# Optimization experiments

Measured on AMD Instinct MI355X. Metric: run time of the kernel, lower is better.

## Reference

```python
import jax, jax.numpy as jnp
import numpy as np

S, Q, N, T, G = 20000, 32, 200000, 30, 64
D_IN, H, D_SV, D_LANG, D_FUSE = 300, 256, 64, 64, 128

def setup_inputs() -> dict:
    key = jax.random.key(0)
    ks = jax.random.split(key, 20)
    sc = 0.05
    inp = {
        'lang_feat': jax.random.normal(ks[0], (Q, T, D_IN), jnp.float32),
        'supvox_feat': jax.random.normal(ks[1], (S, D_SV), jnp.float32),
        'supvox_coords': jax.random.uniform(ks[2], (S, 3), jnp.float32),
        'lang_len': jax.random.randint(ks[3], (Q,), 5, T + 1).astype(jnp.int32),
        'grps': jax.random.randint(ks[4], (S,), 0, G).astype(jnp.int32),
        'supervox': jax.random.randint(ks[5], (N,), 0, S).astype(jnp.int32),
        'gt': jax.random.randint(ks[6], (N, Q), 0, 2).astype(jnp.int32),
        # GRU params (torch layout: [3H, in])
        'gru_w_ih': sc * jax.random.normal(ks[7], (3 * H, D_IN), jnp.float32),
        'gru_w_hh': sc * jax.random.normal(ks[8], (3 * H, H), jnp.float32),
        'gru_b_ih': sc * jax.random.normal(ks[9], (3 * H,), jnp.float32),
        'gru_b_hh': sc * jax.random.normal(ks[10], (3 * H,), jnp.float32),
        # lang_sqz: Linear(256,64) ReLU Linear(64,64)
        'sqz_w1': sc * jax.random.normal(ks[11], (D_LANG, H), jnp.float32),
        'sqz_b1': sc * jax.random.normal(ks[12], (D_LANG,), jnp.float32),
        'sqz_w2': sc * jax.random.normal(ks[13], (D_LANG, D_LANG), jnp.float32),
        'sqz_b2': sc * jax.random.normal(ks[14], (D_LANG,), jnp.float32),
        # feat_fuse: Linear(131,128) ReLU
        'fuse_w': sc * jax.random.normal(ks[15], (D_FUSE, D_SV + 3 + D_LANG), jnp.float32),
        'fuse_b': sc * jax.random.normal(ks[16], (D_FUSE,), jnp.float32),
        # heat_map: Linear(128,2) (Dropout = identity in eval)
        'heat_w': sc * jax.random.normal(ks[17], (2, D_FUSE), jnp.float32),
        'heat_b': sc * jax.random.normal(ks[18], (2,), jnp.float32),
    }
    return inp

def _gru_last(x, lens, w_ih, w_hh, b_ih, b_hh):
    # x: [Q, T, D_IN]; returns hidden at step lens[q]-1 (pack_padded_sequence semantics)
    def step(h, xt_t):
        xt, t = xt_t  # xt: [Q, D_IN]
        gi = xt @ w_ih.T + b_ih          # [Q, 3H]
        gh = h @ w_hh.T + b_hh           # [Q, 3H]
        ir, iz, inn = jnp.split(gi, 3, -1)
        hr, hz, hn = jnp.split(gh, 3, -1)
        r = jax.nn.sigmoid(ir + hr)
        z = jax.nn.sigmoid(iz + hz)
        n = jnp.tanh(inn + r * hn)
        h_new = (1.0 - z) * n + z * h
        h = jnp.where((t < lens)[:, None], h_new, h)
        return h, None
    h0 = jnp.zeros((x.shape[0], w_hh.shape[1]), x.dtype)
    hT, _ = jax.lax.scan(step, h0, (jnp.swapaxes(x, 0, 1), jnp.arange(x.shape[1])))
    return hT  # [Q, H]

def reference(lang_feat, supvox_feat, supvox_coords, lang_len, grps, supervox, gt,
              gru_w_ih, gru_w_hh, gru_b_ih, gru_b_hh,
              sqz_w1, sqz_b1, sqz_w2, sqz_b2, fuse_w, fuse_b, heat_w, heat_b):
    # language branch
    h = _gru_last(lang_feat, lang_len, gru_w_ih, gru_w_hh, gru_b_ih, gru_b_hh)  # [Q,H]
    lang = jax.nn.relu(h @ sqz_w1.T + sqz_b1) @ sqz_w2.T + sqz_b2               # [Q,64]
    # supervoxel branch: cat(feat, coords) -> [S,67]
    sv = jnp.concatenate([supvox_feat, supvox_coords], -1)
    # feat_fuse on cat(sv, lang): split the weight to avoid materializing [S,Q,131]
    d_sv = sv.shape[-1]
    sv_proj = sv @ fuse_w[:, :d_sv].T           # [S,128]
    lang_proj = lang @ fuse_w[:, d_sv:].T       # [Q,128]
    fused = jax.nn.relu(sv_proj[:, None, :] + lang_proj[None, :, :] + fuse_b)  # [S,Q,128]
    logits = fused @ heat_w.T + heat_b          # [S,Q,2]
    obj_score = jax.nn.softmax(logits, -1)[..., 1]  # [S,Q]
    # cluster-grouped mean score (grps_ one-hot; assumes unique(grps)==arange(G))
    grp_oh = (grps[:, None] == jnp.arange(G)).astype(obj_score.dtype)  # [S,G]
    grp_sum = jnp.einsum('sq,sg->qg', obj_score, grp_oh)               # [Q,G]
    sen_grp_score = grp_sum / grp_oh.sum(0)[None, :]                   # [Q,G]
    best = jnp.argmax(sen_grp_score, -1)        # [Q]
    supvox_sen = grp_oh[:, best]                # [S,Q] binary
    obj_pts = supvox_sen[supervox].astype(jnp.int32)  # [N,Q]
    inter = (obj_pts * gt).sum(0).astype(jnp.float32)
    union = jnp.bitwise_or(obj_pts, gt).sum(0).astype(jnp.float32)
    ious = inter / (union + 1e-5)               # [Q]
    return obj_pts, ious
```

## Files before the change

### kernel.cpp

```cpp
#include <hip/hip_runtime.h>
#include <hip/hip_bf16.h>
#include <math.h>

#define S_TOT 20000
#define Q_TOT 32
#define N_TOT 200000
#define T_MAX 30
#define G_TOT 64
#define D_IN 300
#define H_DIM 256
#define D_SV 64
#define D_LANG 64
#define D_FUSE 128
#define D_CAT 67
#define FW_LD 131
#define SCHUNK 32
#define NBLK3 (S_TOT / SCHUNK)
#define SENT64 0xFFFFFFFFFFFFFFFFull
#define OUT_GRID 2048
#define PCHUNK 16
#define PTILES 40

#define GI_MT 32
#define GI_NT 64
#define GI_KC 100
#define GI_NB 12
#define GI_GRID (30 * GI_NB)
#define HG_ELEMS (30 * Q_TOT * H_DIM)

#define SYNCS_N 160

__device__ __forceinline__ float sigmoidf_(float x) { return 1.0f / (1.0f + expf(-x)); }
__device__ __forceinline__ unsigned long long pack2(float a, float b) {
    return ((unsigned long long)__float_as_uint(b) << 32) | (unsigned long long)__float_as_uint(a);
}

__global__ __launch_bounds__(128) void k_gi(const float* __restrict__ lang_feat,
                                            const float* __restrict__ w_ih,
                                            const float* __restrict__ b_ih,
                                            const float* __restrict__ fuse_w,
                                            const float* __restrict__ sqz_w1,
                                            const float* __restrict__ sqz_w2,
                                            const float* __restrict__ heat_w,
                                            float* __restrict__ gi,
                                            float* __restrict__ fwt,
                                            float* __restrict__ w1t,
                                            float* __restrict__ w2t,
                                            float* __restrict__ wdr,
                                            float* __restrict__ hg,
                                            int* __restrict__ syncs) {
    const int tid = threadIdx.x;
    if (blockIdx.x >= GI_GRID) {
        const int xb = blockIdx.x - GI_GRID;
        if (xb == 0) {
            for (int i = tid; i < FW_LD * D_FUSE; i += 128)
                fwt[(i % FW_LD) * D_FUSE + (i / FW_LD)] = fuse_w[i];
            for (int i = tid; i < D_LANG * H_DIM; i += 128)
                w1t[(i & 255) * D_LANG + (i >> 8)] = sqz_w1[i];
            for (int i = tid; i < D_LANG * D_LANG; i += 128)
                w2t[(i & 63) * D_LANG + (i >> 6)] = sqz_w2[i];
            if (tid < D_FUSE) wdr[tid] = heat_w[D_FUSE + tid] - heat_w[tid];
        } else {
            const int fb = xb - 1;
            const int per4 = HG_ELEMS / 4 / 8;
            float4* dst = (float4*)hg + fb * per4;
            const float4 sv = make_float4(__uint_as_float(0xFFFFFFFFu), __uint_as_float(0xFFFFFFFFu),
                                          __uint_as_float(0xFFFFFFFFu), __uint_as_float(0xFFFFFFFFu));
            for (int i = tid; i < per4; i += 128) dst[i] = sv;
            if (fb == 0) for (int i = tid; i < SYNCS_N; i += 128) syncs[i] = 0;
        }
        return;
    }
    __shared__ float x_l[GI_KC][GI_MT + 1];
    __shared__ float w_l[GI_KC][GI_NT + 1];
    const int mb = blockIdx.x / GI_NB, nb = blockIdx.x % GI_NB;
    const int m0 = mb * GI_MT, n0 = nb * GI_NT;
    const int tq4 = (tid >> 4) * 4, jq4 = (tid & 15) * 4;

    float acc[4][4];
    #pragma unroll
    for (int i = 0; i < 4; ++i)
        #pragma unroll
        for (int j = 0; j < 4; ++j) acc[i][j] = 0.f;

    for (int kc = 0; kc < 3; ++kc) {
        const int k0 = kc * GI_KC;
        for (int i = tid; i < GI_MT * GI_KC; i += 128) {
            const int r = i / GI_KC, k = i % GI_KC;
            const int row = m0 + r, q = row / T_MAX, t = row - q * T_MAX;
            x_l[k][r] = lang_feat[(q * T_MAX + t) * D_IN + k0 + k];
        }
        for (int i = tid; i < GI_NT * GI_KC; i += 128) {
            const int r = i / GI_KC, k = i % GI_KC;
            w_l[k][r] = w_ih[(n0 + r) * D_IN + k0 + k];
        }
        __syncthreads();
        #pragma unroll 2
        for (int k = 0; k < GI_KC; ++k) {
            const float x0 = x_l[k][tq4 + 0], x1 = x_l[k][tq4 + 1];
            const float x2 = x_l[k][tq4 + 2], x3 = x_l[k][tq4 + 3];
            const float v0 = w_l[k][jq4 + 0], v1 = w_l[k][jq4 + 1];
            const float v2 = w_l[k][jq4 + 2], v3 = w_l[k][jq4 + 3];
            acc[0][0] = fmaf(x0, v0, acc[0][0]); acc[0][1] = fmaf(x0, v1, acc[0][1]);
            acc[0][2] = fmaf(x0, v2, acc[0][2]); acc[0][3] = fmaf(x0, v3, acc[0][3]);
            acc[1][0] = fmaf(x1, v0, acc[1][0]); acc[1][1] = fmaf(x1, v1, acc[1][1]);
            acc[1][2] = fmaf(x1, v2, acc[1][2]); acc[1][3] = fmaf(x1, v3, acc[1][3]);
            acc[2][0] = fmaf(x2, v0, acc[2][0]); acc[2][1] = fmaf(x2, v1, acc[2][1]);
            acc[2][2] = fmaf(x2, v2, acc[2][2]); acc[2][3] = fmaf(x2, v3, acc[2][3]);
            acc[3][0] = fmaf(x3, v0, acc[3][0]); acc[3][1] = fmaf(x3, v1, acc[3][1]);
            acc[3][2] = fmaf(x3, v2, acc[3][2]); acc[3][3] = fmaf(x3, v3, acc[3][3]);
        }
        __syncthreads();
    }
    const float b0 = b_ih[n0 + jq4 + 0], b1 = b_ih[n0 + jq4 + 1];
    const float b2 = b_ih[n0 + jq4 + 2], b3 = b_ih[n0 + jq4 + 3];
    #pragma unroll
    for (int i = 0; i < 4; ++i) {
        const int row = m0 + tq4 + i;
        const int q = row / T_MAX, t = row - q * T_MAX;
        float4 v = make_float4(acc[i][0] + b0, acc[i][1] + b1, acc[i][2] + b2, acc[i][3] + b3);
        *(float4*)&gi[(q * T_MAX + t) * 768 + n0 + jq4] = v;
    }
}

__global__ __launch_bounds__(384, 1) void k_gru8(const float* __restrict__ gi,
                                                 const float* __restrict__ w_hh,
                                                 const float* __restrict__ b_hh,
                                                 const int* __restrict__ lang_len,
                                                 float* __restrict__ hg,
                                                 float* __restrict__ hbuf,
                                                 const float* __restrict__ w1t,
                                                 const float* __restrict__ b1,
                                                 const float* __restrict__ w2t,
                                                 const float* __restrict__ b2,
                                                 const float* __restrict__ fwt,
                                                 const float* __restrict__ fuse_b,
                                                 float* __restrict__ langc,
                                                 int* __restrict__ qdone) {
    __shared__ __align__(16) float wlds[96 * 256];
    __shared__ __align__(16) float hlq[4 * 68];
    __shared__ float ghl[96];
    __shared__ float gil[T_MAX * 96];

    const int tid = threadIdx.x;
    const int q = blockIdx.x >> 3, b = blockIdx.x & 7;
    int len = lang_len[q]; if (len > T_MAX) len = T_MAX; if (len < 1) len = 1;

    {
        const float4* src4 = (const float4*)w_hh;
        float4* dst4 = (float4*)wlds;
        for (int i = tid; i < 96 * 64; i += 384) {
            const int r = i >> 6, c = i & 63;
            const int grow = ((r >> 5) << 8) + (b << 5) + (r & 31);
            dst4[r * 64 + (c ^ (r & 7))] = src4[grow * 64 + c];
        }
    }
    for (int i = tid; i < len * 96; i += 384) {
        const int t = i / 96, r = i % 96;
        gil[i] = gi[(q * T_MAX + t) * 768 + ((r >> 5) << 8) + (b << 5) + (r & 31)];
    }
    __syncthreads();

    float hfin = 0.f;
    {
        float hnew = 0.f;
        if (tid < 32) {
            const float bhr = b_hh[(b << 5) + tid];
            const float bhz = b_hh[H_DIM + (b << 5) + tid];
            const float bhn = b_hh[2 * H_DIM + (b << 5) + tid];
            const float r = sigmoidf_(gil[tid] + bhr);
            const float z = sigmoidf_(gil[32 + tid] + bhz);
            const float n = tanhf(gil[64 + tid] + r * bhn);
            hnew = (1.f - z) * n;
            if (len == 1) hfin = hnew;
        }
        if (tid < 64 && len > 1) {
            const float a0 = __shfl(hnew, 2 * (tid & 15));
            const float a1 = __shfl(hnew, 2 * (tid & 15) + 1);
            if (tid < 16) {
                unsigned long long* dst = (unsigned long long*)(hg + q * H_DIM + (b << 5));
                __hip_atomic_store(dst + tid, pack2(a0, a1), __ATOMIC_RELAXED, __HIP_MEMORY_SCOPE_AGENT);
            }
        }
    }

    const int row = tid >> 2, ql = tid & 3;
    const float bh = b_hh[((row >> 5) << 8) + (b << 5) + (row & 31)];
    const int rx = row & 7;
    const float4* wrow4 = (const float4*)wlds + row * 64;
    const int cbase = ql << 4;

    for (int t = 1; t < len; ++t) {
        if (tid < 128) {
            const unsigned long long* src =
                (const unsigned long long*)(hg + (size_t)(t - 1) * (Q_TOT * H_DIM) + q * H_DIM);
            unsigned long long v;
            while ((v = __hip_atomic_load(src + tid, __ATOMIC_RELAXED,
                                          __HIP_MEMORY_SCOPE_AGENT)) == SENT64)
                __builtin_amdgcn_s_sleep(1);
            const int k = 2 * tid;
            const int o = (k >> 6) * 68 + (k & 63);
            hlq[o]     = __uint_as_float((unsigned)(v & 0xffffffffu));
            hlq[o + 1] = __uint_as_float((unsigned)(v >> 32));
        }
        __syncthreads();
        float hold = 0.f;
        if (tid < 32) { const int k = (b << 5) + tid; hold = hlq[(k >> 6) * 68 + (k & 63)]; }
        const float4* h4 = (const float4*)(hlq + ql * 68);
        float ax = 0.f, ay = 0.f, az = 0.f, aw = 0.f;
        #pragma unroll
        for (int i = 0; i < 16; ++i) {
            const float4 wv = wrow4[(cbase + i) ^ rx];
            const float4 hv = h4[i];
            ax = fmaf(wv.x, hv.x, ax);
            ay = fmaf(wv.y, hv.y, ay);
            az = fmaf(wv.z, hv.z, az);
            aw = fmaf(wv.w, hv.w, aw);
        }
        float s = (ax + ay) + (az + aw);
        s += __shfl_xor(s, 1);
        s += __shfl_xor(s, 2);
        if (ql == 0) ghl[row] = s + bh;
        __syncthreads();
        float hnew = 0.f;
        if (tid < 32) {
            const float* gt_ = gil + t * 96;
            const float r = sigmoidf_(gt_[tid] + ghl[tid]);
            const float z = sigmoidf_(gt_[32 + tid] + ghl[32 + tid]);
            const float n = tanhf(gt_[64 + tid] + r * ghl[64 + tid]);
            hnew = (1.f - z) * n + z * hold;
            if (t == len - 1) hfin = hnew;
        }
        if (tid < 64 && t < len - 1) {
            const float a0 = __shfl(hnew, 2 * (tid & 15));
            const float a1 = __shfl(hnew, 2 * (tid & 15) + 1);
            if (tid < 16) {
                unsigned long long* dst =
                    (unsigned long long*)(hg + (size_t)t * (Q_TOT * H_DIM) + q * H_DIM + (b << 5));
                __hip_atomic_store(dst + tid, pack2(a0, a1), __ATOMIC_RELAXED, __HIP_MEMORY_SCOPE_AGENT);
            }
        }
    }

    if (tid < 32)
        __hip_atomic_store(&hbuf[q * H_DIM + (b << 5) + tid], hfin,
                           __ATOMIC_RELAXED, __HIP_MEMORY_SCOPE_AGENT);
    asm volatile("s_waitcnt vmcnt(0)" ::: "memory");
    __syncthreads();
    if (tid == 0)
        __hip_atomic_fetch_add(&qdone[q], 1, __ATOMIC_RELAXED, __HIP_MEMORY_SCOPE_AGENT);
    if (b != 0) return;

    if (tid == 0) {
        while (__hip_atomic_load(&qdone[q], __ATOMIC_RELAXED, __HIP_MEMORY_SCOPE_AGENT) < 8)
            __builtin_amdgcn_s_sleep(2);
    }
    __syncthreads();
    float* hql = gil;
    float* t1l = gil + 256;
    float* lgl = gil + 320;
    if (tid < H_DIM)
        hql[tid] = __hip_atomic_load(&hbuf[q * H_DIM + tid], __ATOMIC_RELAXED, __HIP_MEMORY_SCOPE_AGENT);
    __syncthreads();
    if (tid < 256) {
        const int c = tid >> 2, qq = tid & 3;
        float a = 0.f;
        #pragma unroll 8
        for (int j = 0; j < 64; ++j) {
            const int k = (qq << 6) + j;
            a = fmaf(w1t[k * D_LANG + c], hql[k], a);
        }
        a += __shfl_xor(a, 1);
        a += __shfl_xor(a, 2);
        if (qq == 0) t1l[c] = fmaxf(a + b1[c], 0.f);
    }
    __syncthreads();
    if (tid < 256) {
        const int c = tid >> 2, qq = tid & 3;
        float a = 0.f;
        #pragma unroll
        for (int j = 0; j < 16; ++j) {
            const int k = (qq << 4) + j;
            a = fmaf(w2t[k * D_LANG + c], t1l[k], a);
        }
        a += __shfl_xor(a, 1);
        a += __shfl_xor(a, 2);
        if (qq == 0) lgl[c] = a + b2[c];
    }
    __syncthreads();
    if (tid < 256) {
        const int d = tid >> 1, hh = tid & 1;
        float a = 0.f;
        #pragma unroll 8
        for (int j = 0; j < 32; ++j) {
            const int k = (hh << 5) + j;
            a = fmaf(fwt[(D_CAT + k) * D_FUSE + d], lgl[k], a);
        }
        a += __shfl_xor(a, 1);
        if (hh == 0) langc[q * D_FUSE + d] = a + fuse_b[d];
    }
}

__global__ __launch_bounds__(256) void k_fuse(const float* __restrict__ feat,
                                              const float* __restrict__ coords,
                                              const int* __restrict__ grps,
                                              const float* __restrict__ langc,
                                              const float* __restrict__ fwt,
                                              const float* __restrict__ wdr_g,
                                              const float* __restrict__ heat_b,
                                              float* __restrict__ grp_part,
                                              int* __restrict__ cnt_part) {
    __shared__ __align__(16) float svin[SCHUNK][68];
    __shared__ __align__(16) float svp[SCHUNK][132];
    __shared__ float score[SCHUNK][Q_TOT];
    __shared__ int grps_l[SCHUNK];
    const int tid = threadIdx.x;
    const int s0 = blockIdx.x * SCHUNK;

    const int dsl = tid & 7, q = tid >> 3;
    float lc[16], wdr[16];
    #pragma unroll
    for (int i = 0; i < 16; ++i) {
        const int d = dsl * 16 + i;
        lc[i]  = langc[q * D_FUSE + d];
        wdr[i] = wdr_g[d];
    }
    const float hbd = heat_b[1] - heat_b[0];

    for (int i = tid; i < SCHUNK * D_SV; i += 256) {
        const int r = i >> 6, c = i & 63;
        svin[r][c] = feat[(s0 + r) * D_SV + c];
    }
    if (tid < SCHUNK * 3) { const int r = tid / 3, c = tid % 3; svin[r][D_SV + c] = coords[(s0 + r) * 3 + c]; }
    if (tid < SCHUNK) grps_l[tid] = grps[s0 + tid];
    __syncthreads();

    {
        const int d = tid & 127, sl0 = tid >> 7;
        float acc[16];
        #pragma unroll
        for (int i = 0; i < 16; ++i) acc[i] = 0.f;
        for (int k4 = 0; k4 < 16; ++k4) {
            const float w0 = fwt[(4 * k4 + 0) * D_FUSE + d];
            const float w1 = fwt[(4 * k4 + 1) * D_FUSE + d];
            const float w2 = fwt[(4 * k4 + 2) * D_FUSE + d];
            const float w3 = fwt[(4 * k4 + 3) * D_FUSE + d];
            #pragma unroll
            for (int i = 0; i < 16; ++i) {
                const float4 xv = *(const float4*)&svin[sl0 + 2 * i][4 * k4];
                acc[i] = fmaf(xv.x, w0, fmaf(xv.y, w1, fmaf(xv.z, w2, fmaf(xv.w, w3, acc[i]))));
            }
        }
        for (int k = 64; k < D_CAT; ++k) {
            const float wv = fwt[k * D_FUSE + d];
            #pragma unroll
            for (int i = 0; i < 16; ++i)
                acc[i] = fmaf(svin[sl0 + 2 * i][k], wv, acc[i]);
        }
        #pragma unroll
        for (int i = 0; i < 16; ++i) svp[sl0 + 2 * i][d] = acc[i];
    }
    __syncthreads();

    for (int sl = 0; sl < SCHUNK; ++sl) {
        const float4* sv4 = (const float4*)(&svp[sl][dsl * 16]);
        float part = 0.f;
        #pragma unroll
        for (int j = 0; j < 4; ++j) {
            const float4 v = sv4[j];
            part = fmaf(fmaxf(v.x + lc[4*j+0], 0.f), wdr[4*j+0], part);
            part = fmaf(fmaxf(v.y + lc[4*j+1], 0.f), wdr[4*j+1], part);
            part = fmaf(fmaxf(v.z + lc[4*j+2], 0.f), wdr[4*j+2], part);
            part = fmaf(fmaxf(v.w + lc[4*j+3], 0.f), wdr[4*j+3], part);
        }
        part += __shfl_xor(part, 1);
        part += __shfl_xor(part, 2);
        part += __shfl_xor(part, 4);
        if (dsl == 0) score[sl][q] = sigmoidf_(part + hbd);
    }
    __syncthreads();

    for (int i = 0; i < 8; ++i) {
        const int cell = tid + 256 * i;
        const int qq = cell >> 6, g = cell & 63;
        float sum = 0.f;
        #pragma unroll
        for (int sl = 0; sl < SCHUNK; ++sl)
            sum += (grps_l[sl] == g) ? score[sl][qq] : 0.f;
        grp_part[blockIdx.x * (Q_TOT * G_TOT) + cell] = sum;
        if (cell < G_TOT) {
            int c = 0;
            #pragma unroll
            for (int sl = 0; sl < SCHUNK; ++sl) c += (grps_l[sl] == g);
            cnt_part[blockIdx.x * G_TOT + g] = c;
        }
    }
}

__global__ __launch_bounds__(256) void k_post(const float* __restrict__ grp_part,
                                              const int* __restrict__ cnt_part,
                                              const int* __restrict__ grps,
                                              float* __restrict__ grp2,
                                              int* __restrict__ cnt2,
                                              int* __restrict__ best,
                                              int* __restrict__ smask,
                                              int* __restrict__ qtick,
                                              int* __restrict__ gtick) {
    __shared__ float ps[4][G_TOT];
    __shared__ int   pc[4][G_TOT];
    __shared__ float sc[G_TOT];
    __shared__ int bl[Q_TOT];
    __shared__ int myturn, lastq;
    const int tid = threadIdx.x;
    const int q = blockIdx.x & 31, c = blockIdx.x >> 5;
    const int bq = tid >> 6, g = tid & 63;
    const int b0 = c * PTILES;
    int b1 = b0 + PTILES; if (b1 > NBLK3) b1 = NBLK3;

    float acc = 0.f; int cacc = 0;
    for (int b = b0 + bq; b < b1; b += 4) {
        acc  += grp_part[b * (Q_TOT * G_TOT) + q * G_TOT + g];
        cacc += cnt_part[b * G_TOT + g];
    }
    ps[bq][g] = acc; pc[bq][g] = cacc;
    __syncthreads();
    if (tid < G_TOT) {
        const float s = ((ps[0][tid] + ps[1][tid]) + ps[2][tid]) + ps[3][tid];
        const int  cc = ((pc[0][tid] + pc[1][tid]) + pc[2][tid]) + pc[3][tid];
        __hip_atomic_store(&grp2[(c * Q_TOT + q) * G_TOT + tid], s,
                           __ATOMIC_RELAXED, __HIP_MEMORY_SCOPE_AGENT);
        __hip_atomic_store(&cnt2[(c * Q_TOT + q) * G_TOT + tid], cc,
                           __ATOMIC_RELAXED, __HIP_MEMORY_SCOPE_AGENT);
    }
    asm volatile("s_waitcnt vmcnt(0)" ::: "memory");
    if (tid == 0) {
        const int old = __hip_atomic_fetch_add(&qtick[q], 1, __ATOMIC_RELAXED, __HIP_MEMORY_SCOPE_AGENT);
        myturn = (old == PCHUNK - 1) ? 1 : 0;
    }
    __syncthreads();
    if (!myturn) return;

    if (tid < G_TOT) {
        float s = 0.f; int cc = 0;
        #pragma unroll
        for (int c2 = 0; c2 < PCHUNK; ++c2) {
            s  += __hip_atomic_load(&grp2[(c2 * Q_TOT + q) * G_TOT + tid],
                                    __ATOMIC_RELAXED, __HIP_MEMORY_SCOPE_AGENT);
            cc += __hip_atomic_load(&cnt2[(c2 * Q_TOT + q) * G_TOT + tid],
                                    __ATOMIC_RELAXED, __HIP_MEMORY_SCOPE_AGENT);
        }
        sc[tid] = s / (float)cc;
    }
    __syncthreads();
    if (tid == 0) {
        float bv = sc[0]; int bi = 0;
        for (int g2 = 1; g2 < G_TOT; ++g2) if (sc[g2] > bv) { bv = sc[g2]; bi = g2; }
        __hip_atomic_store(&best[q], bi, __ATOMIC_RELAXED, __HIP_MEMORY_SCOPE_AGENT);
        asm volatile("s_waitcnt vmcnt(0)" ::: "memory");
        const int old = __hip_atomic_fetch_add(gtick, 1, __ATOMIC_RELAXED, __HIP_MEMORY_SCOPE_AGENT);
        lastq = (old == Q_TOT - 1) ? 1 : 0;
    }
    __syncthreads();
    if (!lastq) return;
    if (tid < Q_TOT) bl[tid] = __hip_atomic_load(&best[tid], __ATOMIC_RELAXED, __HIP_MEMORY_SCOPE_AGENT);
    __syncthreads();
    for (int s = tid; s < S_TOT; s += 256) {
        const int gg = grps[s];
        int m = 0;
        #pragma unroll
        for (int qq = 0; qq < Q_TOT; ++qq) m |= (bl[qq] == gg) ? (1 << qq) : 0;
        smask[s] = m;
    }
}

__global__ __launch_bounds__(256) void k_out(const int* __restrict__ supervox,
                                             const int* __restrict__ gt,
                                             const int* __restrict__ smask,
                                             float* __restrict__ out,
                                             int* __restrict__ interG, int* __restrict__ unionG,
                                             int* __restrict__ ticket) {
    const int tid = threadIdx.x;
    const int gidx = blockIdx.x * 256 + tid;
    const int q4 = (gidx & 7) * 4;
    const int nstride = (OUT_GRID * 256) >> 3;
    int a0 = 0, a1 = 0, a2 = 0, a3 = 0;
    int u0 = 0, u1 = 0, u2 = 0, u3 = 0;
    for (int n = gidx >> 3; n < N_TOT; n += nstride) {
        const int m = smask[supervox[n]];
        const int4 g4 = *(const int4*)&gt[n * Q_TOT + q4];
        const int o0 = (m >> (q4 + 0)) & 1;
        const int o1 = (m >> (q4 + 1)) & 1;
        const int o2 = (m >> (q4 + 2)) & 1;
        const int o3 = (m >> (q4 + 3)) & 1;
        *(float4*)&out[n * Q_TOT + q4] =
            make_float4((float)o0, (float)o1, (float)o2, (float)o3);
        a0 += o0 & g4.x; u0 += o0 | g4.x;
        a1 += o1 & g4.y; u1 += o1 | g4.y;
        a2 += o2 & g4.z; u2 += o2 | g4.z;
        a3 += o3 & g4.w; u3 += o3 | g4.w;
    }
    __shared__ int bi[Q_TOT], bu[Q_TOT];
    __shared__ int islast;
    if (tid < Q_TOT) { bi[tid] = 0; bu[tid] = 0; }
    __syncthreads();
    atomicAdd(&bi[q4 + 0], a0); atomicAdd(&bu[q4 + 0], u0);
    atomicAdd(&bi[q4 + 1], a1); atomicAdd(&bu[q4 + 1], u1);
    atomicAdd(&bi[q4 + 2], a2); atomicAdd(&bu[q4 + 2], u2);
    atomicAdd(&bi[q4 + 3], a3); atomicAdd(&bu[q4 + 3], u3);
    __syncthreads();
    if (tid < Q_TOT) { atomicAdd(&interG[tid], bi[tid]); atomicAdd(&unionG[tid], bu[tid]); }
    asm volatile("s_waitcnt vmcnt(0)" ::: "memory");
    if (tid == 0) {
        const int old = __hip_atomic_fetch_add(ticket, 1, __ATOMIC_RELAXED, __HIP_MEMORY_SCOPE_AGENT);
        islast = (old == OUT_GRID - 1) ? 1 : 0;
    }
    __syncthreads();
    if (islast && tid < Q_TOT) {
        const int iv = __hip_atomic_load(&interG[tid], __ATOMIC_RELAXED, __HIP_MEMORY_SCOPE_AGENT);
        const int uv = __hip_atomic_load(&unionG[tid], __ATOMIC_RELAXED, __HIP_MEMORY_SCOPE_AGENT);
        out[(size_t)N_TOT * Q_TOT + tid] = (float)iv / ((float)uv + 1e-5f);
    }
}

extern "C" void kernel_launch(void* const* d_in, const int* in_sizes, int n_in,
                              void* d_out, int out_size, void* d_ws, size_t ws_size,
                              hipStream_t stream) {
    const float* lang_feat = (const float*)d_in[0];
    const float* feat      = (const float*)d_in[1];
    const float* coords    = (const float*)d_in[2];
    const int*   lang_len  = (const int*)d_in[3];
    const int*   grps      = (const int*)d_in[4];
    const int*   supervox  = (const int*)d_in[5];
    const int*   gt        = (const int*)d_in[6];
    const float* w_ih      = (const float*)d_in[7];
    const float* w_hh      = (const float*)d_in[8];
    const float* b_ih      = (const float*)d_in[9];
    const float* b_hh      = (const float*)d_in[10];
    const float* sqz_w1    = (const float*)d_in[11];
    const float* sqz_b1    = (const float*)d_in[12];
    const float* sqz_w2    = (const float*)d_in[13];
    const float* sqz_b2    = (const float*)d_in[14];
    const float* fuse_w    = (const float*)d_in[15];
    const float* fuse_b    = (const float*)d_in[16];
    const float* heat_w    = (const float*)d_in[17];
    const float* heat_b    = (const float*)d_in[18];
    float* out = (float*)d_out;

    float* gi       = (float*)d_ws;
    float* hbuf     = gi + 737280;
    float* langc    = hbuf + 8192;
    float* grp_part = langc + 4096;
    int*   cnt_part = (int*)(grp_part + NBLK3 * 2048);
    int*   best     = cnt_part + NBLK3 * 64;
    int*   smask    = best + 32;
    int*   syncs    = smask + S_TOT;
    float* hg       = (float*)(syncs + SYNCS_N);
    float* fwt      = hg + HG_ELEMS;
    float* w1t      = fwt + FW_LD * D_FUSE;
    float* w2t      = w1t + H_DIM * D_LANG;
    float* wdr      = w2t + D_LANG * D_LANG;
    float* grp2     = wdr + 128;
    int*   cnt2     = (int*)(grp2 + PCHUNK * Q_TOT * G_TOT);

    k_gi   <<<GI_GRID + 9, 128, 0, stream>>>(lang_feat, w_ih, b_ih, fuse_w, sqz_w1, sqz_w2, heat_w,
                                             gi, fwt, w1t, w2t, wdr, hg, syncs);
    k_gru8 <<<Q_TOT * 8, 384, 0, stream>>>(gi, w_hh, b_hh, lang_len, hg, hbuf,
                                           w1t, sqz_b1, w2t, sqz_b2, fwt, fuse_b, langc,
                                           syncs + 66);
    k_fuse <<<NBLK3, 256, 0, stream>>>(feat, coords, grps, langc, fwt, wdr, heat_b,
                                       grp_part, cnt_part);
    k_post <<<Q_TOT * PCHUNK, 256, 0, stream>>>(grp_part, cnt_part, grps, grp2, cnt2,
                                                best, smask, syncs + 98, syncs + 65);
    k_out  <<<OUT_GRID, 256, 0, stream>>>(supervox, gt, smask, out, syncs, syncs + 32, syncs + 64);
}
```

Baseline: 249.5 us.

## Fuse fuse, post and output kernels into one persistent kernel with grid barriers

Merges k_fuse, k_post and k_out into a single k_tail kernel of 625 blocks that synchronises its phases through atomic-counter grid barriers (spin-wait with s_sleep) instead of separate launches. The smask computation is spread across all blocks, and the output scatter now uses 625 blocks instead of 2048. The aim is to remove launch gaps and tail effects between the three kernels. It relies on all 625 blocks being co-resident (launch_bounds 256,3) to avoid deadlock, and it adds spin-wait overhead and less parallelism in the output phase.

After: 236.9 us. -5.0%, faster.

```diff
diff --git a/kernel.cpp b/kernel.cpp
--- a/kernel.cpp
+++ b/kernel.cpp
@@ -17,7 +17,6 @@
 #define SCHUNK 32
 #define NBLK3 (S_TOT / SCHUNK)
 #define SENT64 0xFFFFFFFFFFFFFFFFull
-#define OUT_GRID 2048
 #define PCHUNK 16
 #define PTILES 40
 
@@ -33,6 +32,19 @@
 __device__ __forceinline__ float sigmoidf_(float x) { return 1.0f / (1.0f + expf(-x)); }
 __device__ __forceinline__ unsigned long long pack2(float a, float b) {
     return ((unsigned long long)__float_as_uint(b) << 32) | (unsigned long long)__float_as_uint(a);
+}
+__device__ __forceinline__ void tick_wait(int* c, int tgt) {
+    __syncthreads();
+    if (threadIdx.x == 0) {
+        while (__hip_atomic_load(c, __ATOMIC_RELAXED, __HIP_MEMORY_SCOPE_AGENT) < tgt)
+            __builtin_amdgcn_s_sleep(4);
+    }
+    __syncthreads();
+}
+__device__ __forceinline__ void tick_bump(int* c) {
+    asm volatile("s_waitcnt vmcnt(0)" ::: "memory");
+    if (threadIdx.x == 0)
+        __hip_atomic_fetch_add(c, 1, __ATOMIC_RELAXED, __HIP_MEMORY_SCOPE_AGENT);
 }
 
 __global__ __launch_bounds__(128) void k_gi(const float* __restrict__ lang_feat,
@@ -301,224 +313,236 @@
     }
 }
 
-__global__ __launch_bounds__(256) void k_fuse(const float* __restrict__ feat,
-                                              const float* __restrict__ coords,
-                                              const int* __restrict__ grps,
-                                              const float* __restrict__ langc,
-                                              const float* __restrict__ fwt,
-                                              const float* __restrict__ wdr_g,
-                                              const float* __restrict__ heat_b,
-                                              float* __restrict__ grp_part,
-                                              int* __restrict__ cnt_part) {
+__global__ __launch_bounds__(256, 3) void k_tail(const float* __restrict__ feat,
+                                                 const float* __restrict__ coords,
+                                                 const int* __restrict__ grps,
+                                                 const float* __restrict__ langc,
+                                                 const float* __restrict__ fwt,
+                                                 const float* __restrict__ wdr_g,
+                                                 const float* __restrict__ heat_b,
+                                                 float* __restrict__ grp_part,
+                                                 int* __restrict__ cnt_part,
+                                                 float* __restrict__ grp2,
+                                                 int* __restrict__ cnt2,
+                                                 int* __restrict__ best,
+                                                 int* __restrict__ smask,
+                                                 const int* __restrict__ supervox,
+                                                 const int* __restrict__ gt,
+                                                 float* __restrict__ out,
+                                                 int* __restrict__ syncs) {
+    int* interG   = syncs;
+    int* unionG   = syncs + 32;
+    int* t_out    = syncs + 64;
+    int* gtick    = syncs + 65;
+    int* qtick    = syncs + 98;
+    int* t_fuse   = syncs + 130;
+    int* t_smask  = syncs + 131;
+    const int tid = threadIdx.x;
+    const int bid = blockIdx.x;
+
     __shared__ __align__(16) float svin[SCHUNK][68];
     __shared__ __align__(16) float svp[SCHUNK][132];
     __shared__ float score[SCHUNK][Q_TOT];
     __shared__ int grps_l[SCHUNK];
-    const int tid = threadIdx.x;
-    const int s0 = blockIdx.x * SCHUNK;
-
-    const int dsl = tid & 7, q = tid >> 3;
-    float lc[16], wdr[16];
-    #pragma unroll
-    for (int i = 0; i < 16; ++i) {
-        const int d = dsl * 16 + i;
-        lc[i]  = langc[q * D_FUSE + d];
-        wdr[i] = wdr_g[d];
-    }
-    const float hbd = heat_b[1] - heat_b[0];
-
-    for (int i = tid; i < SCHUNK * D_SV; i += 256) {
-        const int r = i >> 6, c = i & 63;
-        svin[r][c] = feat[(s0 + r) * D_SV + c];
-    }
-    if (tid < SCHUNK * 3) { const int r = tid / 3, c = tid % 3; svin[r][D_SV + c] = coords[(s0 + r) * 3 + c]; }
-    if (tid < SCHUNK) grps_l[tid] = grps[s0 + tid];
-    __syncthreads();
-
-    {
-        const int d = tid & 127, sl0 = tid >> 7;
-        float acc[16];
-        #pragma unroll
-        for (int i = 0; i < 16; ++i) acc[i] = 0.f;
-        for (int k4 = 0; k4 < 16; ++k4) {
-            const float w0 = fwt[(4 * k4 + 0) * D_FUSE + d];
-            const float w1 = fwt[(4 * k4 + 1) * D_FUSE + d];
-            const float w2 = fwt[(4 * k4 + 2) * D_FUSE + d];
-            const float w3 = fwt[(4 * k4 + 3) * D_FUSE + d];
-            #pragma unroll
-            for (int i = 0; i < 16; ++i) {
-                const float4 xv = *(const float4*)&svin[sl0 + 2 * i][4 * k4];
-                acc[i] = fmaf(xv.x, w0, fmaf(xv.y, w1, fmaf(xv.z, w2, fmaf(xv.w, w3, acc[i]))));
-            }
-        }
-        for (int k = 64; k < D_CAT; ++k) {
-            const float wv = fwt[k * D_FUSE + d];
-            #pragma unroll
-            for (int i = 0; i < 16; ++i)
-                acc[i] = fmaf(svin[sl0 + 2 * i][k], wv, acc[i]);
-        }
-        #pragma unroll
-        for (int i = 0; i < 16; ++i) svp[sl0 + 2 * i][d] = acc[i];
-    }
-    __syncthreads();
-
-    for (int sl = 0; sl < SCHUNK; ++sl) {
-        const float4* sv4 = (const float4*)(&svp[sl][dsl * 16]);
-        float part = 0.f;
-        #pragma unroll
-        for (int j = 0; j < 4; ++j) {
-            const float4 v = sv4[j];
-            part = fmaf(fmaxf(v.x + lc[4*j+0], 0.f), wdr[4*j+0], part);
-            part = fmaf(fmaxf(v.y + lc[4*j+1], 0.f), wdr[4*j+1], part);
-            part = fmaf(fmaxf(v.z + lc[4*j+2], 0.f), wdr[4*j+2], part);
-            part = fmaf(fmaxf(v.w + lc[4*j+3], 0.f), wdr[4*j+3], part);
-        }
-        part += __shfl_xor(part, 1);
-        part += __shfl_xor(part, 2);
-        part += __shfl_xor(part, 4);
-        if (dsl == 0) score[sl][q] = sigmoidf_(part + hbd);
-    }
-    __syncthreads();
-
-    for (int i = 0; i < 8; ++i) {
-        const int cell = tid + 256 * i;
-        const int qq = cell >> 6, g = cell & 63;
-        float sum = 0.f;
-        #pragma unroll
-        for (int sl = 0; sl < SCHUNK; ++sl)
-            sum += (grps_l[sl] == g) ? score[sl][qq] : 0.f;
-        grp_part[blockIdx.x * (Q_TOT * G_TOT) + cell] = sum;
-        if (cell < G_TOT) {
-            int c = 0;
-            #pragma unroll
-            for (int sl = 0; sl < SCHUNK; ++sl) c += (grps_l[sl] == g);
-            cnt_part[blockIdx.x * G_TOT + g] = c;
-        }
-    }
-}
-
-__global__ __launch_bounds__(256) void k_post(const float* __restrict__ grp_part,
-                                              const int* __restrict__ cnt_part,
-                                              const int* __restrict__ grps,
-                                              float* __restrict__ grp2,
-                                              int* __restrict__ cnt2,
-                                              int* __restrict__ best,
-                                              int* __restrict__ smask,
-                                              int* __restrict__ qtick,
-                                              int* __restrict__ gtick) {
     __shared__ float ps[4][G_TOT];
     __shared__ int   pc[4][G_TOT];
     __shared__ float sc[G_TOT];
     __shared__ int bl[Q_TOT];
-    __shared__ int myturn, lastq;
-    const int tid = threadIdx.x;
-    const int q = blockIdx.x & 31, c = blockIdx.x >> 5;
-    const int bq = tid >> 6, g = tid & 63;
-    const int b0 = c * PTILES;
-    int b1 = b0 + PTILES; if (b1 > NBLK3) b1 = NBLK3;
-
-    float acc = 0.f; int cacc = 0;
-    for (int b = b0 + bq; b < b1; b += 4) {
-        acc  += grp_part[b * (Q_TOT * G_TOT) + q * G_TOT + g];
-        cacc += cnt_part[b * G_TOT + g];
-    }
-    ps[bq][g] = acc; pc[bq][g] = cacc;
-    __syncthreads();
-    if (tid < G_TOT) {
-        const float s = ((ps[0][tid] + ps[1][tid]) + ps[2][tid]) + ps[3][tid];
-        const int  cc = ((pc[0][tid] + pc[1][tid]) + pc[2][tid]) + pc[3][tid];
-        __hip_atomic_store(&grp2[(c * Q_TOT + q) * G_TOT + tid], s,
-                           __ATOMIC_RELAXED, __HIP_MEMORY_SCOPE_AGENT);
-        __hip_atomic_store(&cnt2[(c * Q_TOT + q) * G_TOT + tid], cc,
-                           __ATOMIC_RELAXED, __HIP_MEMORY_SCOPE_AGENT);
-    }
-    asm volatile("s_waitcnt vmcnt(0)" ::: "memory");
-    if (tid == 0) {
-        const int old = __hip_atomic_fetch_add(&qtick[q], 1, __ATOMIC_RELAXED, __HIP_MEMORY_SCOPE_AGENT);
-        myturn = (old == PCHUNK - 1) ? 1 : 0;
-    }
-    __syncthreads();
-    if (!myturn) return;
-
-    if (tid < G_TOT) {
-        float s = 0.f; int cc = 0;
+    __shared__ int bi_s[Q_TOT], bu_s[Q_TOT];
+    __shared__ int islast;
+
+    {
+        const int s0 = bid * SCHUNK;
+        const int dsl = tid & 7, q = tid >> 3;
+        float lc[16], wdr[16];
         #pragma unroll
-        for (int c2 = 0; c2 < PCHUNK; ++c2) {
-            s  += __hip_atomic_load(&grp2[(c2 * Q_TOT + q) * G_TOT + tid],
-                                    __ATOMIC_RELAXED, __HIP_MEMORY_SCOPE_AGENT);
-            cc += __hip_atomic_load(&cnt2[(c2 * Q_TOT + q) * G_TOT + tid],
-                                    __ATOMIC_RELAXED, __HIP_MEMORY_SCOPE_AGENT);
-        }
-        sc[tid] = s / (float)cc;
-    }
-    __syncthreads();
-    if (tid == 0) {
-        float bv = sc[0]; int bi = 0;
-        for (int g2 = 1; g2 < G_TOT; ++g2) if (sc[g2] > bv) { bv = sc[g2]; bi = g2; }
-        __hip_atomic_store(&best[q], bi, __ATOMIC_RELAXED, __HIP_MEMORY_SCOPE_AGENT);
+        for (int i = 0; i < 16; ++i) {
+            const int d = dsl * 16 + i;
+            lc[i]  = langc[q * D_FUSE + d];
+            wdr[i] = wdr_g[d];
+        }
+        const float hbd = heat_b[1] - heat_b[0];
+
+        for (int i = tid; i < SCHUNK * D_SV; i += 256) {
+            const int r = i >> 6, c = i & 63;
+            svin[r][c] = feat[(s0 + r) * D_SV + c];
+        }
+        if (tid < SCHUNK * 3) { const int r = tid / 3, c = tid % 3; svin[r][D_SV + c] = coords[(s0 + r) * 3 + c]; }
+        if (tid < SCHUNK) grps_l[tid] = grps[s0 + tid];
+        __syncthreads();
+
+        {
+            const int d = tid & 127, sl0 = tid >> 7;
+            float acc[16];
+            #pragma unroll
+            for (int i = 0; i < 16; ++i) acc[i] = 0.f;
+            for (int k4 = 0; k4 < 16; ++k4) {
+                const float w0 = fwt[(4 * k4 + 0) * D_FUSE + d];
+                const float w1 = fwt[(4 * k4 + 1) * D_FUSE + d];
+                const float w2 = fwt[(4 * k4 + 2) * D_FUSE + d];
+                const float w3 = fwt[(4 * k4 + 3) * D_FUSE + d];
+                #pragma unroll
+                for (int i = 0; i < 16; ++i) {
+                    const float4 xv = *(const float4*)&svin[sl0 + 2 * i][4 * k4];
+                    acc[i] = fmaf(xv.x, w0, fmaf(xv.y, w1, fmaf(xv.z, w2, fmaf(xv.w, w3, acc[i]))));
+                }
+            }
+            for (int k = 64; k < D_CAT; ++k) {
+                const float wv = fwt[k * D_FUSE + d];
+                #pragma unroll
+                for (int i = 0; i < 16; ++i)
+                    acc[i] = fmaf(svin[sl0 + 2 * i][k], wv, acc[i]);
+            }
+            #pragma unroll
+            for (int i = 0; i < 16; ++i) svp[sl0 + 2 * i][d] = acc[i];
+        }
+        __syncthreads();
+
+        for (int sl = 0; sl < SCHUNK; ++sl) {
+            const float4* sv4 = (const float4*)(&svp[sl][dsl * 16]);
+            float part = 0.f;
+            #pragma unroll
+            for (int j = 0; j < 4; ++j) {
+                const float4 v = sv4[j];
+                part = fmaf(fmaxf(v.x + lc[4*j+0], 0.f), wdr[4*j+0], part);
+                part = fmaf(fmaxf(v.y + lc[4*j+1], 0.f), wdr[4*j+1], part);
+                part = fmaf(fmaxf(v.z + lc[4*j+2], 0.f), wdr[4*j+2], part);
+                part = fmaf(fmaxf(v.w + lc[4*j+3], 0.f), wdr[4*j+3], part);
+            }
+            part += __shfl_xor(part, 1);
+            part += __shfl_xor(part, 2);
+            part += __shfl_xor(part, 4);
+            if (dsl == 0) score[sl][q] = sigmoidf_(part + hbd);
+        }
+        __syncthreads();
+
+        for (int i = 0; i < 8; ++i) {
+            const int cell = tid + 256 * i;
+            const int qq = cell >> 6, g = cell & 63;
+            float sum = 0.f;
+            #pragma unroll
+            for (int sl = 0; sl < SCHUNK; ++sl)
+                sum += (grps_l[sl] == g) ? score[sl][qq] : 0.f;
+            __hip_atomic_store(&grp_part[bid * (Q_TOT * G_TOT) + cell], sum,
+                               __ATOMIC_RELAXED, __HIP_MEMORY_SCOPE_AGENT);
+            if (cell < G_TOT) {
+                int c = 0;
+                #pragma unroll
+                for (int sl = 0; sl < SCHUNK; ++sl) c += (grps_l[sl] == g);
+                __hip_atomic_store(&cnt_part[bid * G_TOT + g], c,
+                                   __ATOMIC_RELAXED, __HIP_MEMORY_SCOPE_AGENT);
+            }
+        }
+        tick_bump(t_fuse);
+    }
+    tick_wait(t_fuse, NBLK3);
+
+    if (bid < Q_TOT * PCHUNK) {
+        const int q = bid & 31, c = bid >> 5;
+        const int bq = tid >> 6, g = tid & 63;
+        const int b0 = c * PTILES;
+        int b1 = b0 + PTILES; if (b1 > NBLK3) b1 = NBLK3;
+        float acc = 0.f; int cacc = 0;
+        for (int b = b0 + bq; b < b1; b += 4) {
+            acc  += __hip_atomic_load(&grp_part[b * (Q_TOT * G_TOT) + q * G_TOT + g],
+                                      __ATOMIC_RELAXED, __HIP_MEMORY_SCOPE_AGENT);
+            cacc += __hip_atomic_load(&cnt_part[b * G_TOT + g],
+                                      __ATOMIC_RELAXED, __HIP_MEMORY_SCOPE_AGENT);
+        }
+        ps[bq][g] = acc; pc[bq][g] = cacc;
+        __syncthreads();
+        if (tid < G_TOT) {
+            const float s = ((ps[0][tid] + ps[1][tid]) + ps[2][tid]) + ps[3][tid];
+            const int  cc = ((pc[0][tid] + pc[1][tid]) + pc[2][tid]) + pc[3][tid];
+            __hip_atomic_store(&grp2[(c * Q_TOT + q) * G_TOT + tid], s,
+                               __ATOMIC_RELAXED, __HIP_MEMORY_SCOPE_AGENT);
+            __hip_atomic_store(&cnt2[(c * Q_TOT + q) * G_TOT + tid], cc,
+                               __ATOMIC_RELAXED, __HIP_MEMORY_SCOPE_AGENT);
+        }
+        __shared__ int myturn;
         asm volatile("s_waitcnt vmcnt(0)" ::: "memory");
-        const int old = __hip_atomic_fetch_add(gtick, 1, __ATOMIC_RELAXED, __HIP_MEMORY_SCOPE_AGENT);
-        lastq = (old == Q_TOT - 1) ? 1 : 0;
-    }
-    __syncthreads();
-    if (!lastq) return;
+        if (tid == 0) {
+            const int old = __hip_atomic_fetch_add(&qtick[q], 1, __ATOMIC_RELAXED, __HIP_MEMORY_SCOPE_AGENT);
+            myturn = (old == PCHUNK - 1) ? 1 : 0;
+        }
+        __syncthreads();
+        if (myturn) {
+            if (tid < G_TOT) {
+                float s = 0.f; int cc = 0;
+                #pragma unroll
+                for (int c2 = 0; c2 < PCHUNK; ++c2) {
+                    s  += __hip_atomic_load(&grp2[(c2 * Q_TOT + q) * G_TOT + tid],
+                                            __ATOMIC_RELAXED, __HIP_MEMORY_SCOPE_AGENT);
+                    cc += __hip_atomic_load(&cnt2[(c2 * Q_TOT + q) * G_TOT + tid],
+                                            __ATOMIC_RELAXED, __HIP_MEMORY_SCOPE_AGENT);
+                }
+                sc[tid] = s / (float)cc;
+            }
+            __syncthreads();
+            if (tid == 0) {
+                float bv = sc[0]; int bi = 0;
+                for (int g2 = 1; g2 < G_TOT; ++g2) if (sc[g2] > bv) { bv = sc[g2]; bi = g2; }
+                __hip_atomic_store(&best[q], bi, __ATOMIC_RELAXED, __HIP_MEMORY_SCOPE_AGENT);
+                asm volatile("s_waitcnt vmcnt(0)" ::: "memory");
+                __hip_atomic_fetch_add(gtick, 1, __ATOMIC_RELAXED, __HIP_MEMORY_SCOPE_AGENT);
+            }
+        }
+    }
+    tick_wait(gtick, Q_TOT);
+
     if (tid < Q_TOT) bl[tid] = __hip_atomic_load(&best[tid], __ATOMIC_RELAXED, __HIP_MEMORY_SCOPE_AGENT);
     __syncthreads();
-    for (int s = tid; s < S_TOT; s += 256) {
+    if (tid < 32) {
+        const int s = bid * 32 + tid;
         const int gg = grps[s];
         int m = 0;
         #pragma unroll
         for (int qq = 0; qq < Q_TOT; ++qq) m |= (bl[qq] == gg) ? (1 << qq) : 0;
-        smask[s] = m;
-    }
-}
-
-__global__ __launch_bounds__(256) void k_out(const int* __restrict__ supervox,
-                                             const int* __restrict__ gt,
-                                             const int* __restrict__ smask,
-                                             float* __restrict__ out,
-                                             int* __restrict__ interG, int* __restrict__ unionG,
-                                             int* __restrict__ ticket) {
-    const int tid = threadIdx.x;
-    const int gidx = blockIdx.x * 256 + tid;
-    const int q4 = (gidx & 7) * 4;
-    const int nstride = (OUT_GRID * 256) >> 3;
-    int a0 = 0, a1 = 0, a2 = 0, a3 = 0;
-    int u0 = 0, u1 = 0, u2 = 0, u3 = 0;
-    for (int n = gidx >> 3; n < N_TOT; n += nstride) {
-        const int m = smask[supervox[n]];
-        const int4 g4 = *(const int4*)&gt[n * Q_TOT + q4];
-        const int o0 = (m >> (q4 + 0)) & 1;
-        const int o1 = (m >> (q4 + 1)) & 1;
-        const int o2 = (m >> (q4 + 2)) & 1;
-        const int o3 = (m >> (q4 + 3)) & 1;
-        *(float4*)&out[n * Q_TOT + q4] =
-            make_float4((float)o0, (float)o1, (float)o2, (float)o3);
-        a0 += o0 & g4.x; u0 += o0 | g4.x;
-        a1 += o1 & g4.y; u1 += o1 | g4.y;
-        a2 += o2 & g4.z; u2 += o2 | g4.z;
-        a3 += o3 & g4.w; u3 += o3 | g4.w;
-    }
-    __shared__ int bi[Q_TOT], bu[Q_TOT];
-    __shared__ int islast;
-    if (tid < Q_TOT) { bi[tid] = 0; bu[tid] = 0; }
-    __syncthreads();
-    atomicAdd(&bi[q4 + 0], a0); atomicAdd(&bu[q4 + 0], u0);
-    atomicAdd(&bi[q4 + 1], a1); atomicAdd(&bu[q4 + 1], u1);
-    atomicAdd(&bi[q4 + 2], a2); atomicAdd(&bu[q4 + 2], u2);
-    atomicAdd(&bi[q4 + 3], a3); atomicAdd(&bu[q4 + 3], u3);
-    __syncthreads();
-    if (tid < Q_TOT) { atomicAdd(&interG[tid], bi[tid]); atomicAdd(&unionG[tid], bu[tid]); }
-    asm volatile("s_waitcnt vmcnt(0)" ::: "memory");
-    if (tid == 0) {
-        const int old = __hip_atomic_fetch_add(ticket, 1, __ATOMIC_RELAXED, __HIP_MEMORY_SCOPE_AGENT);
-        islast = (old == OUT_GRID - 1) ? 1 : 0;
-    }
-    __syncthreads();
-    if (islast && tid < Q_TOT) {
-        const int iv = __hip_atomic_load(&interG[tid], __ATOMIC_RELAXED, __HIP_MEMORY_SCOPE_AGENT);
-        const int uv = __hip_atomic_load(&unionG[tid], __ATOMIC_RELAXED, __HIP_MEMORY_SCOPE_AGENT);
-        out[(size_t)N_TOT * Q_TOT + tid] = (float)iv / ((float)uv + 1e-5f);
+        __hip_atomic_store(&smask[s], m, __ATOMIC_RELAXED, __HIP_MEMORY_SCOPE_AGENT);
+    }
+    tick_bump(t_smask);
+    tick_wait(t_smask, NBLK3);
+
+    {
+        const int gidx = bid * 256 + tid;
+        const int q4 = (gidx & 7) * 4;
+        const int nstride = (NBLK3 * 256) >> 3;
+        int a0 = 0, a1 = 0, a2 = 0, a3 = 0;
+        int u0 = 0, u1 = 0, u2 = 0, u3 = 0;
+        for (int n = gidx >> 3; n < N_TOT; n += nstride) {
+            const int m = __hip_atomic_load(&smask[supervox[n]],
+                                            __ATOMIC_RELAXED, __HIP_MEMORY_SCOPE_AGENT);
+            const int4 g4 = *(const int4*)&gt[n * Q_TOT + q4];
+            const int o0 = (m >> (q4 + 0)) & 1;
+            const int o1 = (m >> (q4 + 1)) & 1;
+            const int o2 = (m >> (q4 + 2)) & 1;
+            const int o3 = (m >> (q4 + 3)) & 1;
+            *(float4*)&out[n * Q_TOT + q4] =
+                make_float4((float)o0, (float)o1, (float)o2, (float)o3);
+            a0 += o0 & g4.x; u0 += o0 | g4.x;
+            a1 += o1 & g4.y; u1 += o1 | g4.y;
+            a2 += o2 & g4.z; u2 += o2 | g4.z;
+            a3 += o3 & g4.w; u3 += o3 | g4.w;
+        }
+        if (tid < Q_TOT) { bi_s[tid] = 0; bu_s[tid] = 0; }
+        __syncthreads();
+        atomicAdd(&bi_s[q4 + 0], a0); atomicAdd(&bu_s[q4 + 0], u0);
+        atomicAdd(&bi_s[q4 + 1], a1); atomicAdd(&bu_s[q4 + 1], u1);
+        atomicAdd(&bi_s[q4 + 2], a2); atomicAdd(&bu_s[q4 + 2], u2);
+        atomicAdd(&bi_s[q4 + 3], a3); atomicAdd(&bu_s[q4 + 3], u3);
+        __syncthreads();
+        if (tid < Q_TOT) { atomicAdd(&interG[tid], bi_s[tid]); atomicAdd(&unionG[tid], bu_s[tid]); }
+        asm volatile("s_waitcnt vmcnt(0)" ::: "memory");
+        if (tid == 0) {
+            const int old = __hip_atomic_fetch_add(t_out, 1, __ATOMIC_RELAXED, __HIP_MEMORY_SCOPE_AGENT);
+            islast = (old == NBLK3 - 1) ? 1 : 0;
+        }
+        __syncthreads();
+        if (islast && tid < Q_TOT) {
+            const int iv = __hip_atomic_load(&interG[tid], __ATOMIC_RELAXED, __HIP_MEMORY_SCOPE_AGENT);
+            const int uv = __hip_atomic_load(&unionG[tid], __ATOMIC_RELAXED, __HIP_MEMORY_SCOPE_AGENT);
+            out[(size_t)N_TOT * Q_TOT + tid] = (float)iv / ((float)uv + 1e-5f);
+        }
     }
 }
 
@@ -567,9 +591,7 @@
     k_gru8 <<<Q_TOT * 8, 384, 0, stream>>>(gi, w_hh, b_hh, lang_len, hg, hbuf,
                                            w1t, sqz_b1, w2t, sqz_b2, fwt, fuse_b, langc,
                                            syncs + 66);
-    k_fuse <<<NBLK3, 256, 0, stream>>>(feat, coords, grps, langc, fwt, wdr, heat_b,
-                                       grp_part, cnt_part);
-    k_post <<<Q_TOT * PCHUNK, 256, 0, stream>>>(grp_part, cnt_part, grps, grp2, cnt2,
-                                                best, smask, syncs + 98, syncs + 65);
-    k_out  <<<OUT_GRID, 256, 0, stream>>>(supervox, gt, smask, out, syncs, syncs + 32, syncs + 64);
-}
+    k_tail <<<NBLK3, 256, 0, stream>>>(feat, coords, grps, langc, fwt, wdr, heat_b,
+                                       grp_part, cnt_part, grp2, cnt2, best, smask,
+                                       supervox, gt, out, syncs);
+}
```
